# Kernel tuning notes

Measured on AMD Instinct MI355X. Metric: run time of the kernel, lower is better.

The kernel has to match this reference:

```python
import jax, jax.numpy as jnp
import numpy as np


def setup_inputs() -> dict:
    key = jax.random.key(0)
    x = jax.random.normal(key, (64, 1024, 1024), dtype=jnp.float32)
    return {"x": x}


def reference(x):
    # x: [B, H, W]
    # finite-difference gradients with zero padding on first row/col
    grad_x = jnp.pad(x[:, :, 1:] - x[:, :, :-1], ((0, 0), (0, 0), (1, 0)))
    grad_y = jnp.pad(x[:, 1:, :] - x[:, :-1, :], ((0, 0), (1, 0), (0, 0)))
    grad_mag = jnp.sqrt(grad_x ** 2 + grad_y ** 2 + 1e-08)

    mean_mag = jnp.mean(grad_mag, axis=(1, 2), keepdims=True)
    edge_density = jnp.mean((grad_mag > mean_mag).astype(x.dtype), axis=(1, 2))
    edge_strength = jnp.mean(grad_mag, axis=(1, 2))
    edge_max = jnp.max(grad_mag, axis=(1, 2))

    grad_angle = jnp.arctan2(grad_y, grad_x + 1e-08)

    pi = np.pi
    angle_feats = []
    for i in range(4):
        a_min = -pi + i * pi / 2
        a_max = -pi + (i + 1) * pi / 2
        mask = (grad_angle >= a_min) & (grad_angle < a_max)
        num = jnp.sum(jnp.where(mask, grad_mag, 0.0), axis=(1, 2))
        den = jnp.sum(mask.astype(x.dtype), axis=(1, 2)) + 1e-08
        angle_feats.append(num / den)
    angle_features = jnp.stack(angle_feats, axis=1)  # [B, 4]

    features = jnp.concatenate(
        [edge_density[:, None], edge_strength[:, None], edge_max[:, None], angle_features],
        axis=1,
    )  # [B, 7]
    return features
```

## Files before the change

kernel.cpp:

```cpp
#include <hip/hip_runtime.h>

#define BATCH 64
#define H 1024
#define W 1024
#define RPB 64
#define STRIPS (H / RPB)
#define NT 256
#define TSHIFT 19
#define TLO 1600
#define NBS 648
#define TBASE 1605
#define NWORDS 4928
#define NFL (NWORDS - TLO)
#define KITERS (NFL / NT)
#define INVN (1.0f / (float)(H * W))

template<bool FIRST>
__device__ __forceinline__ void do_row(const float4 cur, const float4 pv4, float left,
                                       float eps, float& mx2, unsigned int* shWin) {
    float px[4] = {cur.x, cur.y, cur.z, cur.w};
    float pl[4] = {left, cur.x, cur.y, cur.z};
    float pv[4] = {pv4.x, pv4.y, pv4.z, pv4.w};
    #pragma unroll
    for (int j = 0; j < 4; ++j) {
        float gx = px[j] - pl[j];
        float gy = FIRST ? 0.0f : (px[j] - pv[j]);
        float m2 = __builtin_fmaf(gx, gx, __builtin_fmaf(gy, gy, eps));
        mx2 = fmaxf(mx2, m2);
        unsigned int sxp = __float_as_uint(gx) >> 31;
        unsigned int q;
        if (FIRST) {
            q = sxp ? 4u : 0u;
        } else {
            unsigned int sy = __float_as_uint(gy) >> 31;
            q = (sy << 1) | sxp;
        }
        unsigned int widx = q * NBS + (__float_as_uint(m2) >> TSHIFT);
        atomicAdd(&shWin[widx - TLO], 1u);
    }
}

__global__ __launch_bounds__(NT) void pass1_kernel(const float* __restrict__ x,
                                                   unsigned int* __restrict__ hist,
                                                   float* __restrict__ smax) {
    const int strip = blockIdx.x;
    const int b = blockIdx.y;
    const int tid = threadIdx.x;
    const int wave = tid >> 6;
    const int lane = tid & 63;
    const int seg0 = wave << 8;
    const int col = seg0 + (lane << 2);
    const float* img = x + (size_t)b * H * W;
    const int r0 = strip * RPB;
    const int rend = r0 + RPB;
    const float eps = 1e-8f;

    __shared__ unsigned int shWin[NFL];
    __shared__ float shMax[4];

    #pragma unroll
    for (int k = 0; k < KITERS; ++k) shWin[k * NT + tid] = 0u;
    __syncthreads();

    float lb_all = 0.f;
    if (seg0 > 0) lb_all = img[(size_t)(r0 + lane) * W + (seg0 - 1)];

    float mx2 = 0.f;
    float4 prev;
    int r = r0;

    if (r0 == 0) {
        float4 cur0 = *(const float4*)(img + col);
        float sw = __shfl_up(cur0.w, 1, 64);
        float bb = __shfl(lb_all, 0, 64);
        float left = (lane == 0) ? ((seg0 == 0) ? cur0.x : bb) : sw;
        do_row<true>(cur0, cur0, left, eps, mx2, shWin);
        prev = cur0;
        r = 1;
    } else {
        prev = *(const float4*)(img + (size_t)(r0 - 1) * W + col);
    }

    float4 pf0 = *(const float4*)(img + (size_t)r * W + col);
    float4 pf1 = *(const float4*)(img + (size_t)(r + 1) * W + col);
    float4 pf2 = *(const float4*)(img + (size_t)(r + 2) * W + col);
    float4 pf3 = *(const float4*)(img + (size_t)(r + 3) * W + col);

    if ((rend - r) & 1) {
        float4 c0 = pf0;
        pf0 = pf1; pf1 = pf2; pf2 = pf3;
        if (r + 4 < rend) pf3 = *(const float4*)(img + (size_t)(r + 4) * W + col);
        float sw = __shfl_up(c0.w, 1, 64);
        float bb = __shfl(lb_all, r - r0, 64);
        float left = (lane == 0) ? ((seg0 == 0) ? c0.x : bb) : sw;
        do_row<false>(c0, prev, left, eps, mx2, shWin);
        prev = c0;
        ++r;
    }

    for (; r < rend; r += 2) {
        float4 c0 = pf0, c1 = pf1;
        pf0 = pf2; pf1 = pf3;
        if (r + 5 < rend) {
            pf2 = *(const float4*)(img + (size_t)(r + 4) * W + col);
            pf3 = *(const float4*)(img + (size_t)(r + 5) * W + col);
        }
        float sw0 = __shfl_up(c0.w, 1, 64);
        float bb0 = __shfl(lb_all, r - r0, 64);
        float left0 = (lane == 0) ? ((seg0 == 0) ? c0.x : bb0) : sw0;
        float sw1 = __shfl_up(c1.w, 1, 64);
        float bb1 = __shfl(lb_all, r + 1 - r0, 64);
        float left1 = (lane == 0) ? ((seg0 == 0) ? c1.x : bb1) : sw1;
        do_row<false>(c0, prev, left0, eps, mx2, shWin);
        do_row<false>(c1, c0, left1, eps, mx2, shWin);
        prev = c1;
    }

    #pragma unroll
    for (int o = 32; o > 0; o >>= 1)
        mx2 = fmaxf(mx2, __shfl_down(mx2, o, 64));
    if (lane == 0) shMax[wave] = mx2;
    __syncthreads();
    if (tid == 0)
        smax[b * STRIPS + strip] =
            fmaxf(fmaxf(shMax[0], shMax[1]), fmaxf(shMax[2], shMax[3]));

    unsigned int* gh = hist + (size_t)(b * STRIPS + strip) * NFL;
    #pragma unroll
    for (int k = 0; k < KITERS; ++k) gh[k * NT + tid] = shWin[k * NT + tid];
}

__global__ __launch_bounds__(NT) void finalize_kernel(const unsigned int* __restrict__ hist,
                                                      const float* __restrict__ smax,
                                                      float* __restrict__ out) {
    const int b = blockIdx.x;
    const int tid = threadIdx.x;
    const int wv = tid >> 6, ln = tid & 63;
    __shared__ float shRed[4][9];
    __shared__ float shS[4];
    __shared__ float shMean;

    unsigned int acc[KITERS];
    #pragma unroll
    for (int k = 0; k < KITERS; ++k) acc[k] = 0u;
    const unsigned int* basep = hist + (size_t)b * STRIPS * NFL;
    for (int s = 0; s < STRIPS; ++s) {
        const unsigned int* src = basep + (size_t)s * NFL;
        #pragma unroll
        for (int k = 0; k < KITERS; ++k) acc[k] += src[k * NT + tid];
    }

    float mc[KITERS];
    int tt[KITERS], rr[KITERS];
    #pragma unroll
    for (int k = 0; k < KITERS; ++k) {
        int w = k * NT + tid + TLO;
        int d = w - TBASE; d = d < 0 ? 0 : d;
        int q = d / NBS;
        int t = w - q * NBS;
        rr[k] = q; tt[k] = t;
        float lo = __uint_as_float((unsigned int)t << TSHIFT);
        float hi = __uint_as_float((unsigned int)(t + 1) << TSHIFT);
        mc[k] = 0.5f * (sqrtf(lo) + sqrtf(hi));
    }

    float sv = 0.f;
    #pragma unroll
    for (int k = 0; k < KITERS; ++k) sv += (float)acc[k] * mc[k];
    #pragma unroll
    for (int o = 32; o > 0; o >>= 1) sv += __shfl_down(sv, o, 64);
    if (ln == 0) shS[wv] = sv;

    float vm = 0.f;
    if (tid < STRIPS) vm = smax[b * STRIPS + tid];
    if (tid < 64) {
        #pragma unroll
        for (int o = 32; o > 0; o >>= 1)
            vm = fmaxf(vm, __shfl_down(vm, o, 64));
    }
    __syncthreads();
    if (tid == 0) {
        float mean = (shS[0] + shS[1] + shS[2] + shS[3]) * INVN;
        shMean = mean;
        out[b * 7 + 1] = mean;
        out[b * 7 + 2] = sqrtf(vm);
    }
    __syncthreads();
    const float mean = shMean;

    int tmean = (int)(__float_as_uint(mean * mean) >> TSHIFT);
    float lok = sqrtf(__uint_as_float((unsigned int)tmean << TSHIFT));
    float hik = sqrtf(__uint_as_float((unsigned int)(tmean + 1) << TSHIFT));
    float frac = fminf(fmaxf((mean - lok) / (hik - lok), 0.f), 1.f);

    float v[9];
    #pragma unroll
    for (int k = 0; k < 9; ++k) v[k] = 0.f;
    #pragma unroll
    for (int k = 0; k < KITERS; ++k) {
        int rg = rr[k], t = tt[k];
        float h = (float)acc[k];
        float hm = h * mc[k];
        v[0] += (rg == 0) ? hm : 0.f;  v[4] += (rg == 0) ? h : 0.f;
        v[1] += (rg == 1) ? hm : 0.f;  v[5] += (rg == 1) ? h : 0.f;
        v[2] += (rg == 2) ? hm : 0.f;  v[6] += (rg == 2) ? h : 0.f;
        v[3] += (rg == 3) ? hm : 0.f;  v[7] += (rg == 3) ? h : 0.f;
        v[8] += (t > tmean) ? h : ((t == tmean) ? h * (1.f - frac) : 0.f);
    }
    #pragma unroll
    for (int k = 0; k < 9; ++k) {
        #pragma unroll
        for (int o = 32; o > 0; o >>= 1) v[k] += __shfl_down(v[k], o, 64);
    }
    if (ln == 0) {
        #pragma unroll
        for (int k = 0; k < 9; ++k) shRed[wv][k] = v[k];
    }
    __syncthreads();
    if (tid == 0) {
        float t[9];
        #pragma unroll
        for (int k = 0; k < 9; ++k)
            t[k] = shRed[0][k] + shRed[1][k] + shRed[2][k] + shRed[3][k];
        out[b * 7 + 0] = t[8] * INVN;
        out[b * 7 + 3] = t[3] / (t[7] + 1e-8f);
        out[b * 7 + 4] = t[2] / (t[6] + 1e-8f);
        out[b * 7 + 5] = t[0] / (t[4] + 1e-8f);
        out[b * 7 + 6] = t[1] / (t[5] + 1e-8f);
    }
}

extern "C" void kernel_launch(void* const* d_in, const int* in_sizes, int n_in,
                              void* d_out, int out_size, void* d_ws, size_t ws_size,
                              hipStream_t stream) {
    const float* x = (const float*)d_in[0];
    float* out = (float*)d_out;

    unsigned int* hist = (unsigned int*)d_ws;
    float* smax = (float*)(hist + (size_t)BATCH * STRIPS * NFL);

    dim3 grid(STRIPS, BATCH);
    pass1_kernel<<<grid, NT, 0, stream>>>(x, hist, smax);
    finalize_kernel<<<BATCH, NT, 0, stream>>>(hist, smax, out);
}
```

Baseline: 62.05 us.

## Merge per-strip histograms via global atomics and shorten row prefetch

Each strip block now adds its nonzero shared-memory histogram bins straight into a single per-batch global histogram. This replaces the old scheme, where every strip wrote its own copy and the finalize kernel summed sixteen copies. The goal is to cut the workspace write and read-back traffic and to simplify the finalize reduction. The cost is a memset launch and 16-way contended global atomics per bin. The row prefetch in pass1 is also reduced from four rows ahead to two, which lowers register use but hides less load latency.

```diff
diff --git a/kernel.cpp b/kernel.cpp
--- a/kernel.cpp
+++ b/kernel.cpp
@@ -7,12 +7,10 @@
 #define STRIPS (H / RPB)
 #define NT 256
 #define TSHIFT 19
-#define TLO 1600
 #define NBS 648
-#define TBASE 1605
-#define NWORDS 4928
-#define NFL (NWORDS - TLO)
-#define KITERS (NFL / NT)
+#define WBASE 1605
+#define NLDS 3328
+#define KIT (NLDS / NT)
 #define INVN (1.0f / (float)(H * W))
 
 template<bool FIRST>
@@ -36,7 +34,7 @@
             q = (sy << 1) | sxp;
         }
         unsigned int widx = q * NBS + (__float_as_uint(m2) >> TSHIFT);
-        atomicAdd(&shWin[widx - TLO], 1u);
+        atomicAdd(&shWin[widx - WBASE], 1u);
     }
 }
 
@@ -55,11 +53,11 @@
     const int rend = r0 + RPB;
     const float eps = 1e-8f;
 
-    __shared__ unsigned int shWin[NFL];
+    __shared__ unsigned int shWin[NLDS];
     __shared__ float shMax[4];
 
     #pragma unroll
-    for (int k = 0; k < KITERS; ++k) shWin[k * NT + tid] = 0u;
+    for (int k = 0; k < KIT; ++k) shWin[k * NT + tid] = 0u;
     __syncthreads();
 
     float lb_all = 0.f;
@@ -83,13 +81,11 @@
 
     float4 pf0 = *(const float4*)(img + (size_t)r * W + col);
     float4 pf1 = *(const float4*)(img + (size_t)(r + 1) * W + col);
-    float4 pf2 = *(const float4*)(img + (size_t)(r + 2) * W + col);
-    float4 pf3 = *(const float4*)(img + (size_t)(r + 3) * W + col);
 
     if ((rend - r) & 1) {
         float4 c0 = pf0;
-        pf0 = pf1; pf1 = pf2; pf2 = pf3;
-        if (r + 4 < rend) pf3 = *(const float4*)(img + (size_t)(r + 4) * W + col);
+        pf0 = pf1;
+        if (r + 2 < rend) pf1 = *(const float4*)(img + (size_t)(r + 2) * W + col);
         float sw = __shfl_up(c0.w, 1, 64);
         float bb = __shfl(lb_all, r - r0, 64);
         float left = (lane == 0) ? ((seg0 == 0) ? c0.x : bb) : sw;
@@ -100,10 +96,9 @@
 
     for (; r < rend; r += 2) {
         float4 c0 = pf0, c1 = pf1;
-        pf0 = pf2; pf1 = pf3;
-        if (r + 5 < rend) {
-            pf2 = *(const float4*)(img + (size_t)(r + 4) * W + col);
-            pf3 = *(const float4*)(img + (size_t)(r + 5) * W + col);
+        if (r + 3 < rend) {
+            pf0 = *(const float4*)(img + (size_t)(r + 2) * W + col);
+            pf1 = *(const float4*)(img + (size_t)(r + 3) * W + col);
         }
         float sw0 = __shfl_up(c0.w, 1, 64);
         float bb0 = __shfl(lb_all, r - r0, 64);
@@ -125,9 +120,12 @@
         smax[b * STRIPS + strip] =
             fmaxf(fmaxf(shMax[0], shMax[1]), fmaxf(shMax[2], shMax[3]));
 
-    unsigned int* gh = hist + (size_t)(b * STRIPS + strip) * NFL;
-    #pragma unroll
-    for (int k = 0; k < KITERS; ++k) gh[k * NT + tid] = shWin[k * NT + tid];
+    unsigned int* gh = hist + (size_t)b * NLDS;
+    #pragma unroll
+    for (int k = 0; k < KIT; ++k) {
+        unsigned int v = shWin[k * NT + tid];
+        if (v) atomicAdd(&gh[k * NT + tid], v);
+    }
 }
 
 __global__ __launch_bounds__(NT) void finalize_kernel(const unsigned int* __restrict__ hist,
@@ -140,24 +138,18 @@
     __shared__ float shS[4];
     __shared__ float shMean;
 
-    unsigned int acc[KITERS];
-    #pragma unroll
-    for (int k = 0; k < KITERS; ++k) acc[k] = 0u;
-    const unsigned int* basep = hist + (size_t)b * STRIPS * NFL;
-    for (int s = 0; s < STRIPS; ++s) {
-        const unsigned int* src = basep + (size_t)s * NFL;
-        #pragma unroll
-        for (int k = 0; k < KITERS; ++k) acc[k] += src[k * NT + tid];
-    }
-
-    float mc[KITERS];
-    int tt[KITERS], rr[KITERS];
-    #pragma unroll
-    for (int k = 0; k < KITERS; ++k) {
-        int w = k * NT + tid + TLO;
-        int d = w - TBASE; d = d < 0 ? 0 : d;
-        int q = d / NBS;
-        int t = w - q * NBS;
+    unsigned int acc[KIT];
+    const unsigned int* gh = hist + (size_t)b * NLDS;
+    #pragma unroll
+    for (int k = 0; k < KIT; ++k) acc[k] = gh[k * NT + tid];
+
+    float mc[KIT];
+    int tt[KIT], rr[KIT];
+    #pragma unroll
+    for (int k = 0; k < KIT; ++k) {
+        int f = k * NT + tid;
+        int q = f / NBS;
+        int t = f - q * NBS + WBASE;
         rr[k] = q; tt[k] = t;
         float lo = __uint_as_float((unsigned int)t << TSHIFT);
         float hi = __uint_as_float((unsigned int)(t + 1) << TSHIFT);
@@ -166,7 +158,7 @@
 
     float sv = 0.f;
     #pragma unroll
-    for (int k = 0; k < KITERS; ++k) sv += (float)acc[k] * mc[k];
+    for (int k = 0; k < KIT; ++k) sv += (float)acc[k] * mc[k];
     #pragma unroll
     for (int o = 32; o > 0; o >>= 1) sv += __shfl_down(sv, o, 64);
     if (ln == 0) shS[wv] = sv;
@@ -197,7 +189,7 @@
     #pragma unroll
     for (int k = 0; k < 9; ++k) v[k] = 0.f;
     #pragma unroll
-    for (int k = 0; k < KITERS; ++k) {
+    for (int k = 0; k < KIT; ++k) {
         int rg = rr[k], t = tt[k];
         float h = (float)acc[k];
         float hm = h * mc[k];
@@ -237,7 +229,9 @@
     float* out = (float*)d_out;
 
     unsigned int* hist = (unsigned int*)d_ws;
-    float* smax = (float*)(hist + (size_t)BATCH * STRIPS * NFL);
+    float* smax = (float*)(hist + (size_t)BATCH * NLDS);
+
+    hipMemsetAsync(hist, 0, (size_t)BATCH * NLDS * sizeof(unsigned int), stream);
 
     dim3 grid(STRIPS, BATCH);
     pass1_kernel<<<grid, NT, 0, stream>>>(x, hist, smax);
```

New measurement: 59.06 us. 4.8% less time.
